# Kernel tuning notes

Hardware: AMD Instinct MI355X
Metric: run time of the kernel (lower is better)

Reference implementation:

```python
import jax, jax.numpy as jnp
import numpy as np
import math

B, S, HID = 2, 2048, 2048
NH, NKV, HD = 16, 4, 128
N_REP = NH // NKV
THETA = 1000000.0


def apply_rope(x, position_ids, theta=THETA):
    # x: (B, H, S, D), position_ids: (B, S)
    d = x.shape[-1]
    freqs = 1.0 / (theta ** (jnp.arange(0, d, 2, dtype=jnp.float32) / d))  # (D/2,)
    angles = position_ids.astype(jnp.float32)[:, :, None] * freqs[None, None, :]  # (B,S,D/2)
    cos = jnp.cos(angles)[:, None, :, :]  # (B,1,S,D/2)
    sin = jnp.sin(angles)[:, None, :, :]
    x_even = x[..., 0::2]
    x_odd = x[..., 1::2]
    rot_even = x_even * cos - x_odd * sin
    rot_odd = x_even * sin + x_odd * cos
    out = jnp.stack([rot_even, rot_odd], axis=-1)  # (B,H,S,D/2,2)
    return out.reshape(x.shape)


def setup_inputs() -> dict:
    key = jax.random.key(0)
    ks = jax.random.split(key, 6)
    x = jax.random.normal(ks[0], (B, S, HID), dtype=jnp.float32)
    position_ids = jnp.broadcast_to(jnp.arange(S, dtype=jnp.int64)[None, :], (B, S))
    # causal additive mask: 0 on/below diagonal, large negative above
    causal = jnp.where(jnp.tril(jnp.ones((S, S), dtype=bool)), 0.0, -1e9).astype(jnp.float32)
    attention_mask = jnp.broadcast_to(causal[None, None, :, :], (B, 1, S, S))
    sc = 1.0 / math.sqrt(HID)
    Wq = jax.random.normal(ks[1], (HID, NH * HD), dtype=jnp.float32) * sc
    Wk = jax.random.normal(ks[2], (HID, NKV * HD), dtype=jnp.float32) * sc
    Wv = jax.random.normal(ks[3], (HID, NKV * HD), dtype=jnp.float32) * sc
    Wo = jax.random.normal(ks[4], (NH * HD, HID), dtype=jnp.float32) * sc
    return {"x": x, "position_ids": position_ids, "attention_mask": attention_mask,
            "Wq": Wq, "Wk": Wk, "Wv": Wv, "Wo": Wo}


def reference(x, position_ids, attention_mask, Wq, Wk, Wv, Wo):
    b, s, _ = x.shape
    q = (x @ Wq).reshape(b, s, NH, HD).transpose(0, 2, 1, 3)   # (B,NH,S,D)
    k = (x @ Wk).reshape(b, s, NKV, HD).transpose(0, 2, 1, 3)  # (B,NKV,S,D)
    v = (x @ Wv).reshape(b, s, NKV, HD).transpose(0, 2, 1, 3)
    q = apply_rope(q, position_ids)
    k = apply_rope(k, position_ids)
    # repeat_kv: expand KV heads to match Q heads
    k = jnp.repeat(k, N_REP, axis=1)  # (B,NH,S,D)
    v = jnp.repeat(v, N_REP, axis=1)
    scale = 1.0 / math.sqrt(HD)
    scores = jnp.einsum('bhqd,bhkd->bhqk', q, k) * scale
    scores = scores + attention_mask
    attn = jax.nn.softmax(scores, axis=-1)
    out = jnp.einsum('bhqk,bhkd->bhqd', attn, v)
    out = out.transpose(0, 2, 1, 3).reshape(b, s, NH * HD)
    return out @ Wo
```

## Files before the change

### kernel.cpp

```cpp
#include <hip/hip_runtime.h>
#include <hip/hip_bf16.h>

#define S_LEN 2048
#define HID_D 2048
#define NH 16
#define NKV 4
#define HD 128
#define BATCH 2

typedef __hip_bfloat16 bf16;
using f32x4 = __attribute__((ext_vector_type(4))) float;
using s16x8 = __attribute__((ext_vector_type(8))) short;

struct TrueT { static constexpr bool value = true; };
struct FalseT { static constexpr bool value = false; };

__device__ __forceinline__ f32x4 mfma_16x16x32(s16x8 a, s16x8 b, f32x4 c) {
  return __builtin_amdgcn_mfma_f32_16x16x32_bf16(a, b, c, 0, 0, 0);
}

__device__ __forceinline__ void gload16(const void* g, void* l) {
  __builtin_amdgcn_global_load_lds(
      (const __attribute__((address_space(1))) void*)g,
      (__attribute__((address_space(3))) void*)l, 16, 0, 0);
}

__device__ __forceinline__ unsigned int pk2bf(float a, float b) {
  __hip_bfloat16 lo = __float2bfloat16(a), hi = __float2bfloat16(b);
  return ((unsigned int)*(unsigned short*)&hi << 16) | *(unsigned short*)&lo;
}

__global__ __launch_bounds__(256) void convert_bf16_k(const float* __restrict__ in,
                                                      bf16* __restrict__ out) {
  int i = (blockIdx.x * 256 + threadIdx.x) * 4;
  float4 v = *(const float4*)&in[i];
  out[i + 0] = __float2bfloat16(v.x);
  out[i + 1] = __float2bfloat16(v.y);
  out[i + 2] = __float2bfloat16(v.z);
  out[i + 3] = __float2bfloat16(v.w);
}

__global__ __launch_bounds__(256) void transpose_convert_k(const float* __restrict__ in,
                                                           bf16* __restrict__ out,
                                                           int K, int N) {
  __shared__ float tile[32][33];
  int n0 = blockIdx.x * 32, k0 = blockIdx.y * 32;
  int tx = threadIdx.x, ty = threadIdx.y;
#pragma unroll
  for (int i = ty; i < 32; i += 8) tile[i][tx] = in[(size_t)(k0 + i) * N + n0 + tx];
  __syncthreads();
#pragma unroll
  for (int i = ty; i < 32; i += 8)
    out[(size_t)(n0 + i) * K + k0 + tx] = __float2bfloat16(tile[tx][i]);
}

__global__ __launch_bounds__(512) void gemm256_k(const bf16* __restrict__ A,
                                                 const bf16* __restrict__ Bt,
                                                 bf16* __restrict__ C,
                                                 int M, int N, int K) {
  __shared__ bf16 Asm[2][256 * 64];
  __shared__ bf16 Bsm[2][256 * 64];
  const int tid = threadIdx.x;
  const int lane = tid & 63, wid = tid >> 6;
  const int fr = lane & 15, hi = lane >> 4;

  const int bid = blockIdx.y * gridDim.x + blockIdx.x;
  const int nwg = gridDim.x * gridDim.y;
  const int swz = (bid & 7) * (nwg >> 3) + (bid >> 3);
  const int m0 = (swz % gridDim.x) * 256;
  const int n0 = (swz / gridDim.x) * 256;

  const bf16* Ag = A + (size_t)m0 * K;
  const bf16* Bg = Bt + (size_t)n0 * K;

  auto stageT = [&](const bf16* src, bf16* ldsBase, int k0) {
#pragma unroll
    for (int c = 0; c < 4; ++c) {
      int byte = tid * 16 + c * 8192;
      int row = byte >> 7;
      int col = byte & 127;
      int colSw = col ^ ((row & 7) << 4);
      gload16((const char*)(src + (size_t)row * K + k0) + colSw,
              (char*)ldsBase + byte);
    }
  };

  f32x4 acc[4][8];
#pragma unroll
  for (int m = 0; m < 4; ++m)
#pragma unroll
    for (int n = 0; n < 8; ++n) acc[m][n] = (f32x4){0.f, 0.f, 0.f, 0.f};

  const int r0 = (wid >> 1) * 64;
  const int c0 = (wid & 1) * 128;
  const int NT = K >> 6;

  stageT(Ag, &Asm[0][0], 0);
  stageT(Bg, &Bsm[0][0], 0);
  asm volatile("s_waitcnt vmcnt(0)" ::: "memory");
  __builtin_amdgcn_s_barrier();

  for (int t = 0; t < NT; ++t) {
    const int cur = t & 1;
    const int nxt = cur ^ 1;
    const int kn = (t + 1) << 6;
    const bool more = (t + 1) < NT;
#pragma unroll
    for (int p = 0; p < 2; ++p) {
      s16x8 af[4], bq[8];
#pragma unroll
      for (int m = 0; m < 4; ++m) {
        int r = r0 + m * 16 + fr;
        int cb = (p * 64 + hi * 16) ^ ((r & 7) << 4);
        af[m] = *(const s16x8*)((const char*)&Asm[cur][0] + r * 128 + cb);
      }
#pragma unroll
      for (int n = 0; n < 8; ++n) {
        int bn = c0 + n * 16 + fr;
        int cb = (p * 64 + hi * 16) ^ ((bn & 7) << 4);
        bq[n] = *(const s16x8*)((const char*)&Bsm[cur][0] + bn * 128 + cb);
      }
      if (p == 0) {
        if (more) {
          stageT(Ag, &Asm[nxt][0], kn);
          stageT(Bg, &Bsm[nxt][0], kn);
        }
      } else {
        asm volatile("s_waitcnt vmcnt(0)" ::: "memory");
      }
      __builtin_amdgcn_s_barrier();

      __builtin_amdgcn_s_setprio(1);
#pragma unroll
      for (int m = 0; m < 4; ++m)
#pragma unroll
        for (int n = 0; n < 8; ++n)
          acc[m][n] = mfma_16x16x32(af[m], bq[n], acc[m][n]);
      __builtin_amdgcn_s_setprio(0);
    }
  }

#pragma unroll
  for (int m = 0; m < 4; ++m)
#pragma unroll
    for (int n = 0; n < 8; ++n) {
      const int row = m0 + r0 + m * 16 + hi * 4;
      const int col = n0 + c0 + n * 16 + fr;
#pragma unroll
      for (int r = 0; r < 4; ++r)
        C[(size_t)(row + r) * N + col] = __float2bfloat16(acc[m][n][r]);
    }
}

__global__ __launch_bounds__(256) void gemm128sq_k(const bf16* __restrict__ A,
                                                   const bf16* __restrict__ Bt,
                                                   float* __restrict__ C,
                                                   int M, int N, int K) {
  __shared__ bf16 Asm[2][128 * 64];
  __shared__ bf16 Bsm[2][128 * 64];
  const int tid = threadIdx.x;
  const int lane = tid & 63, wid = tid >> 6;
  const int fr = lane & 15, hi = lane >> 4;

  const int bid = blockIdx.y * gridDim.x + blockIdx.x;
  const int nwg = gridDim.x * gridDim.y;
  const int swz = (bid & 7) * (nwg >> 3) + (bid >> 3);
  const int m0 = (swz % gridDim.x) * 128;
  const int n0 = (swz / gridDim.x) * 128;

  const bf16* Ag = A + (size_t)m0 * K;
  const bf16* Bg = Bt + (size_t)n0 * K;

  auto stageT = [&](const bf16* src, bf16* ldsBase, int k0) {
#pragma unroll
    for (int c = 0; c < 4; ++c) {
      int byte = tid * 16 + c * 4096;
      int row = byte >> 7;
      int col = byte & 127;
      int colSw = col ^ ((row & 7) << 4);
      gload16((const char*)(src + (size_t)row * K + k0) + colSw,
              (char*)ldsBase + byte);
    }
  };

  f32x4 acc[4][4];
#pragma unroll
  for (int m = 0; m < 4; ++m)
#pragma unroll
    for (int n = 0; n < 4; ++n) acc[m][n] = (f32x4){0.f, 0.f, 0.f, 0.f};

  const int r0 = (wid >> 1) * 64;
  const int c0 = (wid & 1) * 64;
  const int NT = K >> 6;

  stageT(Ag, &Asm[0][0], 0);
  stageT(Bg, &Bsm[0][0], 0);
  asm volatile("s_waitcnt vmcnt(0)" ::: "memory");
  __builtin_amdgcn_s_barrier();

  for (int t = 0; t < NT; ++t) {
    const int cur = t & 1;
    const int nxt = cur ^ 1;
    const int kn = (t + 1) << 6;
    const bool more = (t + 1) < NT;
#pragma unroll
    for (int p = 0; p < 2; ++p) {
      s16x8 af[4], bq[4];
#pragma unroll
      for (int m = 0; m < 4; ++m) {
        int r = r0 + m * 16 + fr;
        int cb = (p * 64 + hi * 16) ^ ((r & 7) << 4);
        af[m] = *(const s16x8*)((const char*)&Asm[cur][0] + r * 128 + cb);
      }
#pragma unroll
      for (int n = 0; n < 4; ++n) {
        int bn = c0 + n * 16 + fr;
        int cb = (p * 64 + hi * 16) ^ ((bn & 7) << 4);
        bq[n] = *(const s16x8*)((const char*)&Bsm[cur][0] + bn * 128 + cb);
      }
      if (p == 0) {
        if (more) {
          stageT(Ag, &Asm[nxt][0], kn);
          stageT(Bg, &Bsm[nxt][0], kn);
        }
      } else {
        asm volatile("s_waitcnt vmcnt(0)" ::: "memory");
      }
      __builtin_amdgcn_s_barrier();

      __builtin_amdgcn_s_setprio(1);
#pragma unroll
      for (int m = 0; m < 4; ++m)
#pragma unroll
        for (int n = 0; n < 4; ++n)
          acc[m][n] = mfma_16x16x32(af[m], bq[n], acc[m][n]);
      __builtin_amdgcn_s_setprio(0);
    }
  }

#pragma unroll
  for (int m = 0; m < 4; ++m)
#pragma unroll
    for (int n = 0; n < 4; ++n) {
      const int row = m0 + r0 + m * 16 + hi * 4;
      const int col = n0 + c0 + n * 16 + fr;
#pragma unroll
      for (int r = 0; r < 4; ++r)
        C[(size_t)(row + r) * N + col] = acc[m][n][r];
    }
}

__global__ __launch_bounds__(256) void rope_q_k(const bf16* __restrict__ qkv,
                                                const int* __restrict__ pos_ids,
                                                bf16* __restrict__ Q) {
  int idx = blockIdx.x * 256 + threadIdx.x;
  int i = idx & 63;
  int h = (idx >> 6) & 15;
  int s = (idx >> 10) & 2047;
  int b = idx >> 21;
  const float kscale = 0.12751841418861862f;
  float pos = (float)pos_ids[b * S_LEN + s];
  float freq = exp2f((float)i * -0.31143075889569023f);
  float ang = pos * freq;
  float sn, cs;
  sincosf(ang, &sn, &cs);
  const bf16* src = qkv + (size_t)(b * S_LEN + s) * 3072 + h * HD + 2 * i;
  float e = __bfloat162float(src[0]), o = __bfloat162float(src[1]);
  bf16* dst = Q + ((size_t)(b * NH + h) * S_LEN + s) * HD + 2 * i;
  dst[0] = __float2bfloat16((e * cs - o * sn) * kscale);
  dst[1] = __float2bfloat16((e * sn + o * cs) * kscale);
}

__global__ __launch_bounds__(256) void rope_k_k(const bf16* __restrict__ qkv,
                                                const int* __restrict__ pos_ids,
                                                bf16* __restrict__ Kd) {
  int idx = blockIdx.x * 256 + threadIdx.x;
  int i = idx & 63;
  int kvh = (idx >> 6) & 3;
  int s = (idx >> 8) & 2047;
  int b = idx >> 19;
  float pos = (float)pos_ids[b * S_LEN + s];
  float freq = exp2f((float)i * -0.31143075889569023f);
  float ang = pos * freq;
  float sn, cs;
  sincosf(ang, &sn, &cs);
  const bf16* src = qkv + (size_t)(b * S_LEN + s) * 3072 + 2048 + kvh * HD + 2 * i;
  float e = __bfloat162float(src[0]), o = __bfloat162float(src[1]);
  bf16* dst = Kd + ((size_t)(b * NKV + kvh) * S_LEN + s) * HD + 2 * i;
  dst[0] = __float2bfloat16(e * cs - o * sn);
  dst[1] = __float2bfloat16(e * sn + o * cs);
}

__global__ __launch_bounds__(256) void v_trans_k(const bf16* __restrict__ qkv,
                                                 bf16* __restrict__ Vt) {
  __shared__ unsigned short tile[32][33];
  const int tx = threadIdx.x, ty = threadIdx.y;
  const int s0 = blockIdx.x * 32;
  const int d0 = blockIdx.y * 32;
  const int b = blockIdx.z >> 2, kvh = blockIdx.z & 3;
  const unsigned short* src = (const unsigned short*)qkv + 2560 + kvh * HD;
#pragma unroll
  for (int i = ty; i < 32; i += 8)
    tile[i][tx] = src[(size_t)(b * S_LEN + s0 + i) * 3072 + d0 + tx];
  __syncthreads();
  unsigned short* dst = (unsigned short*)Vt + (size_t)(b * NKV + kvh) * HD * S_LEN;
#pragma unroll
  for (int i = ty; i < 32; i += 8)
    dst[(size_t)(d0 + i) * S_LEN + s0 + tx] = tile[tx][i];
}

__global__ __launch_bounds__(256) void attn_k(const bf16* __restrict__ Q,
                                              const bf16* __restrict__ K,
                                              const bf16* __restrict__ Vt,
                                              bf16* __restrict__ Aout) {
  __shared__ bf16 Ks[2][64 * 128];
  __shared__ bf16 Vs[2][128 * 64];
  __shared__ bf16 Ps[4][16 * 64];

  const int lane = threadIdx.x & 63;
  const int wid = threadIdx.x >> 6;
  const int fr = lane & 15;
  const int hi = lane >> 4;
  const int pi = blockIdx.x, h = blockIdx.y, b = blockIdx.z;
  const int kvh = h >> 2;
  const bf16* Qh = Q + (size_t)(b * NH + h) * S_LEN * HD;
  const bf16* Kh = K + (size_t)(b * NKV + kvh) * S_LEN * HD;
  const bf16* Vh = Vt + (size_t)(b * NKV + kvh) * HD * S_LEN;

  const int oB = lane * 16;
  const int rinK = oB >> 8;
  const int rinV = oB >> 7;
  bf16* myP = &Ps[wid][0];
  const int pswz = (fr & 7) << 4;

  auto stageKV = [&](int bufi, int kv0) {
#pragma unroll
    for (int c = 0; c < 4; ++c) {
      int absr = wid * 16 + c * 4 + rinK;
      int colb = (oB & 255) ^ (((absr >> 2) & 7) << 4);
      gload16((const char*)Kh + (size_t)(kv0 + absr) * 256 + colb,
              (char*)&Ks[bufi][0] + (wid * 16 + c * 4) * 256);
    }
#pragma unroll
    for (int c = 0; c < 4; ++c) {
      int absd = wid * 32 + c * 8 + rinV;
      int colb = (oB & 127) ^ ((absd & 7) << 4);
      gload16((const char*)Vh + (size_t)absd * (S_LEN * 2) + (size_t)kv0 * 2 + colb,
              (char*)&Vs[bufi][0] + (wid * 32 + c * 8) * 128);
    }
  };

#pragma unroll 1
  for (int t = 0; t < 2; ++t) {
    const int qb = t ? (31 - pi) : pi;
    const int q0w = qb * 64 + wid * 16;
    const int nsteps = qb + 1;

    s16x8 qf[4];
#pragma unroll
    for (int ks = 0; ks < 4; ++ks)
      qf[ks] = *(const s16x8*)&Qh[(size_t)(q0w + fr) * HD + ks * 32 + hi * 8];

    f32x4 o[8];
#pragma unroll
    for (int ds = 0; ds < 8; ++ds) o[ds] = (f32x4){0.f, 0.f, 0.f, 0.f};
    float lacc[4];
#pragma unroll
    for (int r = 0; r < 4; ++r) lacc[r] = 0.f;

    auto doStep = [&](int kv0, int bufc, auto LASTC) {
      constexpr bool LAST = decltype(LASTC)::value;
      f32x4 sg[4];
#pragma unroll
      for (int kv = 0; kv < 4; ++kv) {
        f32x4 a = (f32x4){0.f, 0.f, 0.f, 0.f};
        const int row = 4 * fr + kv;
#pragma unroll
        for (int ks = 0; ks < 4; ++ks) {
          int cb = (ks * 64 + hi * 16) ^ (((row >> 2) & 7) << 4);
          s16x8 kf = *(const s16x8*)((const char*)&Ks[bufc][0] + row * 256 + cb);
          a = mfma_16x16x32(qf[ks], kf, a);
        }
        sg[kv] = a;
      }

#pragma unroll
      for (int r = 0; r < 4; ++r) {
        float p0 = __builtin_exp2f(sg[0][r]);
        float p1 = __builtin_exp2f(sg[1][r]);
        float p2 = __builtin_exp2f(sg[2][r]);
        float p3 = __builtin_exp2f(sg[3][r]);
        if (LAST) {
          const int qrow = q0w + hi * 4 + r;
          const int kb = kv0 + 4 * fr;
          p0 = (kb <= qrow) ? p0 : 0.f;
          p1 = (kb + 1 <= qrow) ? p1 : 0.f;
          p2 = (kb + 2 <= qrow) ? p2 : 0.f;
          p3 = (kb + 3 <= qrow) ? p3 : 0.f;
        }
        lacc[r] += (p0 + p1) + (p2 + p3);
        const int prow = hi * 4 + r;
        uint2 pv;
        pv.x = pk2bf(p0, p1);
        pv.y = pk2bf(p2, p3);
        *(uint2*)((char*)myP + prow * 128 + ((fr * 8) ^ ((prow & 7) << 4))) = pv;
      }
      __builtin_amdgcn_wave_barrier();

      s16x8 pf[2];
#pragma unroll
      for (int g = 0; g < 2; ++g) {
        int cb = (g * 64 + hi * 16) ^ pswz;
        pf[g] = *(const s16x8*)((const char*)myP + fr * 128 + cb);
      }
      __builtin_amdgcn_wave_barrier();
#pragma unroll
      for (int ds = 0; ds < 8; ++ds) {
#pragma unroll
        for (int g = 0; g < 2; ++g) {
          int d = ds * 16 + fr;
          int cb = (g * 64 + hi * 16) ^ ((d & 7) << 4);
          s16x8 vf = *(const s16x8*)((const char*)&Vs[bufc][0] + d * 128 + cb);
          o[ds] = mfma_16x16x32(pf[g], vf, o[ds]);
        }
      }
    };

    int buf = 0;
    stageKV(0, 0);
    __syncthreads();

    for (int s = 0; s < nsteps - 1; ++s) {
      stageKV(buf ^ 1, s * 64 + 64);
      doStep(s * 64, buf, FalseT{});
      __syncthreads();
      buf ^= 1;
    }
    doStep((nsteps - 1) * 64, buf, TrueT{});
    __syncthreads();

#pragma unroll
    for (int r = 0; r < 4; ++r) {
      float l = lacc[r];
      l += __shfl_xor(l, 1, 16);
      l += __shfl_xor(l, 2, 16);
      l += __shfl_xor(l, 4, 16);
      l += __shfl_xor(l, 8, 16);
      float inv = 1.0f / l;
      const int srow = q0w + hi * 4 + r;
      bf16* orow = Aout + ((size_t)b * S_LEN + srow) * HID_D + h * HD;
#pragma unroll
      for (int ds = 0; ds < 8; ++ds)
        orow[ds * 16 + fr] = __float2bfloat16(o[ds][r] * inv);
    }
  }
}

extern "C" void kernel_launch(void* const* d_in, const int* in_sizes, int n_in,
                              void* d_out, int out_size, void* d_ws, size_t ws_size,
                              hipStream_t stream) {
  const float* x = (const float*)d_in[0];
  const int* pos = (const int*)d_in[1];
  const float* Wq = (const float*)d_in[3];
  const float* Wk = (const float*)d_in[4];
  const float* Wv = (const float*)d_in[5];
  const float* Wo = (const float*)d_in[6];
  float* out = (float*)d_out;

  char* ws = (char*)d_ws;
  size_t off = 0;
  auto alloc = [&](size_t bytes) {
    char* p = ws + off;
    off += (bytes + 255) & ~(size_t)255;
    return p;
  };
  bf16* xb = (bf16*)alloc((size_t)4096 * 2048 * 2);
  bf16* WqkvT = (bf16*)alloc((size_t)3072 * 2048 * 2);
  bf16* WoT = (bf16*)alloc((size_t)2048 * 2048 * 2);
  bf16* qkv = (bf16*)alloc((size_t)4096 * 3072 * 2);
  bf16* Qb = (bf16*)alloc((size_t)BATCH * NH * S_LEN * HD * 2);
  bf16* Kb = (bf16*)alloc((size_t)BATCH * NKV * S_LEN * HD * 2);
  bf16* Vtb = (bf16*)alloc((size_t)BATCH * NKV * HD * S_LEN * 2);
  bf16* aout = (bf16*)qkv;

  convert_bf16_k<<<8192, 256, 0, stream>>>(x, xb);
  dim3 tb(32, 8);
  transpose_convert_k<<<dim3(64, 64), tb, 0, stream>>>(Wq, WqkvT, 2048, 2048);
  transpose_convert_k<<<dim3(16, 64), tb, 0, stream>>>(Wk, WqkvT + (size_t)2048 * 2048, 2048, 512);
  transpose_convert_k<<<dim3(16, 64), tb, 0, stream>>>(Wv, WqkvT + (size_t)2560 * 2048, 2048, 512);
  transpose_convert_k<<<dim3(64, 64), tb, 0, stream>>>(Wo, WoT, 2048, 2048);

  gemm256_k<<<dim3(16, 12), 512, 0, stream>>>(xb, WqkvT, qkv, 4096, 3072, 2048);

  rope_q_k<<<16384, 256, 0, stream>>>(qkv, pos, Qb);
  rope_k_k<<<4096, 256, 0, stream>>>(qkv, pos, Kb);
  v_trans_k<<<dim3(64, 4, 8), tb, 0, stream>>>(qkv, Vtb);

  attn_k<<<dim3(16, NH, BATCH), 256, 0, stream>>>(Qb, Kb, Vtb, aout);

  gemm128sq_k<<<dim3(32, 16), 256, 0, stream>>>(aout, WoT, out, 4096, 2048, 2048);
}
```

Before: 200.5 us.

## Restructure causal attention into 8-wave blocks with 32-row waves and 32-key steps

Reworks the attention kernel so each 512-thread block handles a complementary pair of 128-row query blocks. Each wave now owns 32 query rows, so every K and V fragment read from LDS feeds two MFMAs, halving LDS traffic per MFMA. KV steps shrink to 32 keys. K is staged into padded LDS rows instead of XOR-swizzled ones, and V is prefetched through registers and written to LDS after compute. Risks: waves in the lower query block sit idle for many steps, the loop needs more barriers per unit of work, and register pressure is higher.

```diff
diff --git a/kernel.cpp b/kernel.cpp
--- a/kernel.cpp
+++ b/kernel.cpp
@@ -11,9 +11,6 @@
 typedef __hip_bfloat16 bf16;
 using f32x4 = __attribute__((ext_vector_type(4))) float;
 using s16x8 = __attribute__((ext_vector_type(8))) short;
-
-struct TrueT { static constexpr bool value = true; };
-struct FalseT { static constexpr bool value = false; };
 
 __device__ __forceinline__ f32x4 mfma_16x16x32(s16x8 a, s16x8 b, f32x4 c) {
   return __builtin_amdgcn_mfma_f32_16x16x32_bf16(a, b, c, 0, 0, 0);
@@ -309,151 +306,144 @@
     dst[(size_t)(d0 + i) * S_LEN + s0 + tx] = tile[tx][i];
 }
 
-__global__ __launch_bounds__(256) void attn_k(const bf16* __restrict__ Q,
+__global__ __launch_bounds__(512) void attn_k(const bf16* __restrict__ Q,
                                               const bf16* __restrict__ K,
                                               const bf16* __restrict__ Vt,
                                               bf16* __restrict__ Aout) {
-  __shared__ bf16 Ks[2][64 * 128];
-  __shared__ bf16 Vs[2][128 * 64];
-  __shared__ bf16 Ps[4][16 * 64];
-
-  const int lane = threadIdx.x & 63;
-  const int wid = threadIdx.x >> 6;
-  const int fr = lane & 15;
-  const int hi = lane >> 4;
+  __shared__ __align__(16) char KsB[2][8320];
+  __shared__ __align__(16) char VsB[2][10240];
+  __shared__ __align__(16) char PsB[8][2560];
+
+  const int tid = threadIdx.x;
+  const int lane = tid & 63, wid = tid >> 6;
+  const int fr = lane & 15, hi = lane >> 4;
   const int pi = blockIdx.x, h = blockIdx.y, b = blockIdx.z;
   const int kvh = h >> 2;
   const bf16* Qh = Q + (size_t)(b * NH + h) * S_LEN * HD;
   const bf16* Kh = K + (size_t)(b * NKV + kvh) * S_LEN * HD;
   const bf16* Vh = Vt + (size_t)(b * NKV + kvh) * HD * S_LEN;
 
-  const int oB = lane * 16;
-  const int rinK = oB >> 8;
-  const int rinV = oB >> 7;
-  bf16* myP = &Ps[wid][0];
-  const int pswz = (fr & 7) << 4;
-
-  auto stageKV = [&](int bufi, int kv0) {
-#pragma unroll
-    for (int c = 0; c < 4; ++c) {
-      int absr = wid * 16 + c * 4 + rinK;
-      int colb = (oB & 255) ^ (((absr >> 2) & 7) << 4);
-      gload16((const char*)Kh + (size_t)(kv0 + absr) * 256 + colb,
-              (char*)&Ks[bufi][0] + (wid * 16 + c * 4) * 256);
-    }
-#pragma unroll
-    for (int c = 0; c < 4; ++c) {
-      int absd = wid * 32 + c * 8 + rinV;
-      int colb = (oB & 127) ^ ((absd & 7) << 4);
-      gload16((const char*)Vh + (size_t)absd * (S_LEN * 2) + (size_t)kv0 * 2 + colb,
-              (char*)&Vs[bufi][0] + (wid * 32 + c * 8) * 128);
-    }
+  const int qb = (wid < 4) ? pi : (15 - pi);
+  const int q0w = qb * 128 + (wid & 3) * 32;
+  const int nsteps = 4 * (15 - pi) + 4;
+
+  s16x8 qf[2][4];
+#pragma unroll
+  for (int u = 0; u < 2; ++u)
+#pragma unroll
+    for (int ks = 0; ks < 4; ++ks)
+      qf[u][ks] = *(const s16x8*)&Qh[(size_t)(q0w + u * 16 + fr) * HD + ks * 32 + hi * 8];
+
+  f32x4 o[2][8];
+#pragma unroll
+  for (int u = 0; u < 2; ++u)
+#pragma unroll
+    for (int ds = 0; ds < 8; ++ds) o[u][ds] = (f32x4){0.f, 0.f, 0.f, 0.f};
+  float lacc[2][4];
+#pragma unroll
+  for (int u = 0; u < 2; ++u)
+#pragma unroll
+    for (int r = 0; r < 4; ++r) lacc[u][r] = 0.f;
+
+  auto stageK = [&](int bufi, int kv0) {
+    gload16((const char*)Kh + ((size_t)(kv0 + wid * 4)) * 256 + lane * 16,
+            &KsB[bufi][0] + wid * 1040);
   };
-
-#pragma unroll 1
-  for (int t = 0; t < 2; ++t) {
-    const int qb = t ? (31 - pi) : pi;
-    const int q0w = qb * 64 + wid * 16;
-    const int nsteps = qb + 1;
-
-    s16x8 qf[4];
-#pragma unroll
-    for (int ks = 0; ks < 4; ++ks)
-      qf[ks] = *(const s16x8*)&Qh[(size_t)(q0w + fr) * HD + ks * 32 + hi * 8];
-
-    f32x4 o[8];
-#pragma unroll
-    for (int ds = 0; ds < 8; ++ds) o[ds] = (f32x4){0.f, 0.f, 0.f, 0.f};
-    float lacc[4];
-#pragma unroll
-    for (int r = 0; r < 4; ++r) lacc[r] = 0.f;
-
-    auto doStep = [&](int kv0, int bufc, auto LASTC) {
-      constexpr bool LAST = decltype(LASTC)::value;
-      f32x4 sg[4];
-#pragma unroll
-      for (int kv = 0; kv < 4; ++kv) {
-        f32x4 a = (f32x4){0.f, 0.f, 0.f, 0.f};
-        const int row = 4 * fr + kv;
+  const int vd = tid >> 2;
+  const int vko = (tid & 3) * 8;
+  auto vload = [&](int kv0) {
+    return *(const s16x8*)&Vh[(size_t)vd * S_LEN + kv0 + vko];
+  };
+
+  stageK(0, 0);
+  {
+    s16x8 v0 = vload(0);
+    *(s16x8*)(&VsB[0][0] + vd * 80 + (tid & 3) * 16) = v0;
+  }
+  __syncthreads();
+
+  int buf = 0;
+  for (int s = 0; s < nsteps; ++s) {
+    const int kv0 = s * 32;
+    const bool more = (s + 1) < nsteps;
+    s16x8 vnext = {};
+    if (more) {
+      stageK(buf ^ 1, kv0 + 32);
+      vnext = vload(kv0 + 32);
+    }
+
+    if (kv0 <= q0w) {
+      const bool diag = (kv0 == q0w);
+      f32x4 sg[2][2];
+#pragma unroll
+      for (int u = 0; u < 2; ++u)
+#pragma unroll
+        for (int kv = 0; kv < 2; ++kv) sg[u][kv] = (f32x4){0.f, 0.f, 0.f, 0.f};
+#pragma unroll
+      for (int kv = 0; kv < 2; ++kv) {
+        const int row = 2 * fr + kv;
+        const char* kbase = &KsB[buf][0] + (row >> 2) * 1040 + (row & 3) * 256;
 #pragma unroll
         for (int ks = 0; ks < 4; ++ks) {
-          int cb = (ks * 64 + hi * 16) ^ (((row >> 2) & 7) << 4);
-          s16x8 kf = *(const s16x8*)((const char*)&Ks[bufc][0] + row * 256 + cb);
-          a = mfma_16x16x32(qf[ks], kf, a);
+          s16x8 kf = *(const s16x8*)(kbase + ks * 64 + hi * 16);
+          sg[0][kv] = mfma_16x16x32(qf[0][ks], kf, sg[0][kv]);
+          sg[1][kv] = mfma_16x16x32(qf[1][ks], kf, sg[1][kv]);
         }
-        sg[kv] = a;
-      }
-
-#pragma unroll
-      for (int r = 0; r < 4; ++r) {
-        float p0 = __builtin_exp2f(sg[0][r]);
-        float p1 = __builtin_exp2f(sg[1][r]);
-        float p2 = __builtin_exp2f(sg[2][r]);
-        float p3 = __builtin_exp2f(sg[3][r]);
-        if (LAST) {
-          const int qrow = q0w + hi * 4 + r;
-          const int kb = kv0 + 4 * fr;
-          p0 = (kb <= qrow) ? p0 : 0.f;
-          p1 = (kb + 1 <= qrow) ? p1 : 0.f;
-          p2 = (kb + 2 <= qrow) ? p2 : 0.f;
-          p3 = (kb + 3 <= qrow) ? p3 : 0.f;
+      }
+
+#pragma unroll
+      for (int u = 0; u < 2; ++u)
+#pragma unroll
+        for (int r = 0; r < 4; ++r) {
+          float p0 = __builtin_exp2f(sg[u][0][r]);
+          float p1 = __builtin_exp2f(sg[u][1][r]);
+          if (diag) {
+            const int qrow = u * 16 + hi * 4 + r;
+            p0 = (2 * fr <= qrow) ? p0 : 0.f;
+            p1 = (2 * fr + 1 <= qrow) ? p1 : 0.f;
+          }
+          lacc[u][r] += p0 + p1;
+          const int prow = u * 16 + hi * 4 + r;
+          *(unsigned int*)(&PsB[wid][0] + prow * 80 + fr * 4) = pk2bf(p0, p1);
         }
-        lacc[r] += (p0 + p1) + (p2 + p3);
-        const int prow = hi * 4 + r;
-        uint2 pv;
-        pv.x = pk2bf(p0, p1);
-        pv.y = pk2bf(p2, p3);
-        *(uint2*)((char*)myP + prow * 128 + ((fr * 8) ^ ((prow & 7) << 4))) = pv;
-      }
       __builtin_amdgcn_wave_barrier();
 
       s16x8 pf[2];
 #pragma unroll
-      for (int g = 0; g < 2; ++g) {
-        int cb = (g * 64 + hi * 16) ^ pswz;
-        pf[g] = *(const s16x8*)((const char*)myP + fr * 128 + cb);
-      }
+      for (int u = 0; u < 2; ++u)
+        pf[u] = *(const s16x8*)(&PsB[wid][0] + (u * 16 + fr) * 80 + hi * 16);
       __builtin_amdgcn_wave_barrier();
+
 #pragma unroll
       for (int ds = 0; ds < 8; ++ds) {
-#pragma unroll
-        for (int g = 0; g < 2; ++g) {
-          int d = ds * 16 + fr;
-          int cb = (g * 64 + hi * 16) ^ ((d & 7) << 4);
-          s16x8 vf = *(const s16x8*)((const char*)&Vs[bufc][0] + d * 128 + cb);
-          o[ds] = mfma_16x16x32(pf[g], vf, o[ds]);
-        }
-      }
-    };
-
-    int buf = 0;
-    stageKV(0, 0);
+        s16x8 vf = *(const s16x8*)(&VsB[buf][0] + (ds * 16 + fr) * 80 + hi * 16);
+        o[0][ds] = mfma_16x16x32(pf[0], vf, o[0][ds]);
+        o[1][ds] = mfma_16x16x32(pf[1], vf, o[1][ds]);
+      }
+    }
+
+    if (more)
+      *(s16x8*)(&VsB[buf ^ 1][0] + vd * 80 + (tid & 3) * 16) = vnext;
     __syncthreads();
-
-    for (int s = 0; s < nsteps - 1; ++s) {
-      stageKV(buf ^ 1, s * 64 + 64);
-      doStep(s * 64, buf, FalseT{});
-      __syncthreads();
-      buf ^= 1;
-    }
-    doStep((nsteps - 1) * 64, buf, TrueT{});
-    __syncthreads();
-
+    buf ^= 1;
+  }
+
+#pragma unroll
+  for (int u = 0; u < 2; ++u)
 #pragma unroll
     for (int r = 0; r < 4; ++r) {
-      float l = lacc[r];
+      float l = lacc[u][r];
       l += __shfl_xor(l, 1, 16);
       l += __shfl_xor(l, 2, 16);
       l += __shfl_xor(l, 4, 16);
       l += __shfl_xor(l, 8, 16);
       float inv = 1.0f / l;
-      const int srow = q0w + hi * 4 + r;
+      const int srow = q0w + u * 16 + hi * 4 + r;
       bf16* orow = Aout + ((size_t)b * S_LEN + srow) * HID_D + h * HD;
 #pragma unroll
       for (int ds = 0; ds < 8; ++ds)
-        orow[ds * 16 + fr] = __float2bfloat16(o[ds][r] * inv);
-    }
-  }
+        orow[ds * 16 + fr] = __float2bfloat16(o[u][ds][r] * inv);
+    }
 }
 
 extern "C" void kernel_launch(void* const* d_in, const int* in_sizes, int n_in,
@@ -496,7 +486,7 @@
   rope_k_k<<<4096, 256, 0, stream>>>(qkv, pos, Kb);
   v_trans_k<<<dim3(64, 4, 8), tb, 0, stream>>>(qkv, Vtb);
 
-  attn_k<<<dim3(16, NH, BATCH), 256, 0, stream>>>(Qb, Kb, Vtb, aout);
+  attn_k<<<dim3(8, NH, BATCH), 512, 0, stream>>>(Qb, Kb, Vtb, aout);
 
   gemm128sq_k<<<dim3(32, 16), 256, 0, stream>>>(aout, WoT, out, 4096, 2048, 2048);
 }
```

After: 233.9 us. 1.17x slower.
